# Performance work log

Measured on AMD Instinct MI355X. Metric: run time of the kernel, lower is better.

## Reference

```python
import jax, jax.numpy as jnp
import numpy as np

EMBED_DIM = 512
N_HEADS = 8
HEAD_DIM = EMBED_DIM // N_HEADS
SEQ = 4096
BATCH = 2


def setup_inputs() -> dict:
    key = jax.random.key(0)
    k1, k2, k3 = jax.random.split(key, 3)
    x = jax.random.normal(k1, (SEQ, BATCH, EMBED_DIM), dtype=jnp.float32)
    # xavier_uniform for [3E, E]: limit = sqrt(6/(3E+E))
    lim_in = float(np.sqrt(6.0 / (3 * EMBED_DIM + EMBED_DIM)))
    in_proj_weight = jax.random.uniform(k2, (3 * EMBED_DIM, EMBED_DIM), minval=-lim_in, maxval=lim_in, dtype=jnp.float32)
    in_proj_bias = jnp.zeros((3 * EMBED_DIM,), jnp.float32)
    lim_out = float(np.sqrt(1.0 / EMBED_DIM))  # torch Linear default init range
    out_weight = jax.random.uniform(k3, (EMBED_DIM, EMBED_DIM), minval=-lim_out, maxval=lim_out, dtype=jnp.float32)
    out_bias = jnp.zeros((EMBED_DIM,), jnp.float32)
    return {"x": x, "in_proj_weight": in_proj_weight, "in_proj_bias": in_proj_bias,
            "out_weight": out_weight, "out_bias": out_bias}


def reference(x, in_proj_weight, in_proj_bias, out_weight, out_bias):
    # x: [S, B, E] (seq-first, as in the torch module)
    S, B, E = x.shape
    H, D = N_HEADS, HEAD_DIM
    scaling = 1.0 / (D ** 0.5)
    qkv = x @ in_proj_weight.T + in_proj_bias            # [S, B, 3E]
    q, k, v = jnp.split(qkv, 3, axis=-1)                 # each [S, B, E]
    # reshape to [B*H, S, D]
    def to_bh(t):
        return t.reshape(S, B * H, D).transpose(1, 0, 2)
    q = to_bh(q * scaling)
    k = to_bh(k)
    v = to_bh(v)
    scores = jnp.einsum('bqd,bkd->bqk', q, k)            # [B*H, S, S]
    attn = jax.nn.softmax(scores, axis=-1)
    out = jnp.einsum('bqk,bkd->bqd', attn, v)            # [B*H, S, D]
    out = out.transpose(1, 0, 2).reshape(S, B, E)        # [S, B, E]
    return out @ out_weight.T + out_bias
```

## Files before the change

kernel.cpp:

```cpp
#include <hip/hip_runtime.h>

typedef unsigned short u16;
typedef unsigned int   u32;
typedef short bf16x8 __attribute__((ext_vector_type(8)));
typedef float f32x2  __attribute__((ext_vector_type(2)));
typedef float f32x4  __attribute__((ext_vector_type(4)));
typedef float f32x16 __attribute__((ext_vector_type(16)));
typedef u32   u32x4  __attribute__((ext_vector_type(4)));

#define QK_SCALE 0.18033688011112042f

__device__ __forceinline__ u16 f2bf(float f) {
  u32 u = __builtin_bit_cast(u32, f);
  u = (u + 0x7FFFu + ((u >> 16) & 1u)) >> 16;
  return (u16)u;
}

__device__ __forceinline__ u32 cvtpk(float lo, float hi) {
  u32 r;
  asm("v_cvt_pk_bf16_f32 %0, %1, %2" : "=v"(r) : "v"(lo), "v"(hi));
  return r;
}

__device__ __forceinline__ void gload16(void* lds, const void* g) {
  __builtin_amdgcn_global_load_lds(
      (const __attribute__((address_space(1))) u32*)g,
      (__attribute__((address_space(3))) u32*)lds, 16, 0, 0);
}

__device__ __forceinline__ bf16x8 ld8(const void* p) {
  return *(const bf16x8*)p;
}

__global__ __launch_bounds__(256) void cvt_kernel(
    const float* __restrict__ x, const float* __restrict__ w1,
    const float* __restrict__ w2,
    u16* __restrict__ xb, u16* __restrict__ wb, u16* __restrict__ ob) {
  int i = blockIdx.x * 256 + threadIdx.x;
  const float* src; u16* dst; int off;
  if (i < 1048576)            { src = x;  dst = xb; off = i; }
  else if (i < 1048576+196608){ src = w1; dst = wb; off = i - 1048576; }
  else                        { src = w2; dst = ob; off = i - 1245184; }
  float4 v = ((const float4*)src)[off];
  ushort4 o;
  o.x = f2bf(v.x); o.y = f2bf(v.y); o.z = f2bf(v.z); o.w = f2bf(v.w);
  ((ushort4*)dst)[off] = o;
}

template<int MODE>
__global__ __launch_bounds__(256, 2) void gemm_bt(
    const u16* __restrict__ A, const u16* __restrict__ Bm,
    const float* __restrict__ bias,
    u16* __restrict__ q_out, u16* __restrict__ k_out, u16* __restrict__ v_out,
    float* __restrict__ f_out, int M, int N, int K) {
  __shared__ __attribute__((aligned(16))) u16 As[128 * 64];
  __shared__ __attribute__((aligned(16))) u16 Bs[128 * 64];
  const int tid = threadIdx.x, lane = tid & 63, w = tid >> 6;
  const int wm = w >> 1, wn = w & 1;
  const int lo = lane & 15, hi = lane >> 4;
  const int m0 = blockIdx.x * 128, n0 = blockIdx.y * 128;
  f32x4 acc[4][4] = {};
  const int srow = lane >> 3;
  const int skc  = (lane & 7) ^ srow;
  const int nk = K >> 6;
  for (int kt = 0; kt < nk; ++kt) {
    __syncthreads();
    const int k0 = kt * 64;
#pragma unroll
    for (int c = 0; c < 4; ++c) {
      const int ch = w * 4 + c;
      const int row = ch * 8 + srow;
      gload16((char*)As + ch * 1024, A  + (size_t)(m0 + row) * K + k0 + skc * 8);
      gload16((char*)Bs + ch * 1024, Bm + (size_t)(n0 + row) * K + k0 + skc * 8);
    }
    __syncthreads();
#pragma unroll
    for (int kk = 0; kk < 2; ++kk) {
      bf16x8 af[4], bfr[4];
#pragma unroll
      for (int mi = 0; mi < 4; ++mi) {
        const int row = wm * 64 + mi * 16 + lo;
        const int kc = kk * 4 + hi;
        af[mi] = ld8((const char*)As + row * 128 + ((kc ^ (row & 7)) << 4));
      }
#pragma unroll
      for (int ni = 0; ni < 4; ++ni) {
        const int row = wn * 64 + ni * 16 + lo;
        const int kc = kk * 4 + hi;
        bfr[ni] = ld8((const char*)Bs + row * 128 + ((kc ^ (row & 7)) << 4));
      }
#pragma unroll
      for (int mi = 0; mi < 4; ++mi)
#pragma unroll
        for (int ni = 0; ni < 4; ++ni)
          acc[mi][ni] = __builtin_amdgcn_mfma_f32_16x16x32_bf16(
              af[mi], bfr[ni], acc[mi][ni], 0, 0, 0);
    }
  }
#pragma unroll
  for (int mi = 0; mi < 4; ++mi)
#pragma unroll
    for (int ni = 0; ni < 4; ++ni) {
      const int gn = n0 + wn * 64 + ni * 16 + lo;
      const float bv = bias[gn];
#pragma unroll
      for (int r = 0; r < 4; ++r) {
        const int gm = m0 + wm * 64 + mi * 16 + hi * 4 + r;
        float val = acc[mi][ni][r] + bv;
        if (MODE == 0) {
          const int s = gm >> 1, b = gm & 1;
          const int sec = gn >> 9, e = gn & 511;
          const int h = e >> 6, d = e & 63;
          const size_t o = (((size_t)(b * 8 + h) * 4096 + s) << 6) + d;
          if (sec == 0)      q_out[o] = f2bf(val * QK_SCALE);
          else if (sec == 1) k_out[o] = f2bf(val);
          else               v_out[o] = f2bf(val);
        } else {
          f_out[(size_t)gm * N + gn] = val;
        }
      }
    }
}

__global__ __launch_bounds__(256) void transpose_v(
    const u16* __restrict__ v, u16* __restrict__ vt) {
  __shared__ __attribute__((aligned(16))) u16 T[64 * 72];
  const int bh = blockIdx.y, s0 = blockIdx.x * 64;
  const int t = threadIdx.x;
#pragma unroll
  for (int i = 0; i < 2; ++i) {
    const int idx = t + i * 256;
    const int row = idx >> 3, c = idx & 7;
    uint4 d = *(const uint4*)(v + ((size_t)bh * 4096 + s0 + row) * 64 + c * 8);
    *(uint4*)(&T[row * 72 + c * 8]) = d;
  }
  __syncthreads();
#pragma unroll
  for (int i = 0; i < 2; ++i) {
    const int idx = t + i * 256;
    const int dcol = idx >> 3, sc = idx & 7;
    u16 tmp[8];
#pragma unroll
    for (int j = 0; j < 8; ++j) tmp[j] = T[(sc * 8 + j) * 72 + dcol];
    *(uint4*)(vt + ((size_t)bh * 64 + dcol) * 4096 + s0 + sc * 8) = *(const uint4*)tmp;
  }
}

__global__ __launch_bounds__(256, 2) void fa_kernel(
    const u16* __restrict__ q, const u16* __restrict__ k,
    const u16* __restrict__ vt, u16* __restrict__ attn) {
  __shared__ __attribute__((aligned(16))) char S_lds[2][2][16384];
  __shared__ float Ml[2][2][32];
  const int tid = threadIdx.x, lane = tid & 63, w = tid >> 6;
  const int lo = lane & 31, hi5 = lane >> 5;
  const int wq = w & 1;
  const int kvh = w >> 1;
  const int wg = blockIdx.x;
  const int xcd = wg & 7, idx = wg >> 3;
  const int bh = xcd * 2 + (idx >> 5), qb = idx & 31;
  const int q0 = qb * 128 + wq * 64;
  const size_t hb = (size_t)bh * 4096 * 64;
  const u16* kbase = k + hb;
  const u16* vbase = vt + hb;
  bf16x8 qfA[4], qfB[4];
#pragma unroll
  for (int ds = 0; ds < 4; ++ds) {
    qfA[ds] = ld8(q + hb + (size_t)(q0 + lo) * 64 + ds * 16 + hi5 * 8);
    qfB[ds] = ld8(q + hb + (size_t)(q0 + 32 + lo) * 64 + ds * 16 + hi5 * 8);
  }

  f32x16 accA[2] = {}, accB[2] = {};
  float lrunA = 0.f, lrunB = 0.f;

  const int srow8 = lane >> 3;
  const int sx    = (lane & 7) ^ srow8;
  const int schunk = wq * 4;

#define STAGE(buf, kv0)                                                       \
  {                                                                           \
    char* kb_l = S_lds[kvh][buf];                                             \
    char* vb_l = kb_l + 8192;                                                 \
    _Pragma("unroll")                                                         \
    for (int i = 0; i < 4; ++i) {                                             \
      const int c = schunk + i;                       \
      gload16(kb_l + c * 1024,                                                \
              kbase + (size_t)((kv0) + c * 8 + srow8) * 64 + sx * 8);         \
      gload16(vb_l + c * 1024,                                                \
              vbase + (size_t)(c * 8 + srow8) * 4096 + (kv0) + sx * 8);       \
    }                                                                         \
  }

#define PACK(stv, ksl, pa)                                                    \
  {                                                                           \
    u32 A0 = cvtpk(stv[8 * ksl + 0], stv[8 * ksl + 1]);                       \
    u32 A1 = cvtpk(stv[8 * ksl + 2], stv[8 * ksl + 3]);                       \
    u32 B0 = cvtpk(stv[8 * ksl + 4], stv[8 * ksl + 5]);                       \
    u32 B1 = cvtpk(stv[8 * ksl + 6], stv[8 * ksl + 7]);                       \
    asm("v_permlane32_swap_b32 %0, %1" : "+v"(A0), "+v"(B0));                 \
    asm("v_permlane32_swap_b32 %0, %1" : "+v"(A1), "+v"(B1));                 \
    u32x4 pw; pw.x = A0; pw.y = A1; pw.z = B0; pw.w = B1;                     \
    pa = __builtin_bit_cast(bf16x8, pw);                                      \
  }

  const int kvbase = kvh * 2048;
  STAGE(0, kvbase);
  __syncthreads();

  for (int kb = 0; kb < 32; ++kb) {
    const int cur = kb & 1;
    if (kb < 31) STAGE(cur ^ 1, kvbase + (kb + 1) * 64);
    const char* kl = S_lds[kvh][cur];
    const char* vl = kl + 8192;
    f32x16 stA0 = {}, stA1 = {}, stB0 = {}, stB1 = {};
    __builtin_amdgcn_s_setprio(1);
#pragma unroll
    for (int ds = 0; ds < 4; ++ds) {
      const int r0 = lo, r1 = 32 + lo;
      const int col = ds * 32 + hi5 * 16;
      bf16x8 kf0 = ld8(kl + r0 * 128 + (col ^ ((r0 & 7) << 4)));
      bf16x8 kf1 = ld8(kl + r1 * 128 + (col ^ ((r1 & 7) << 4)));
      stA0 = __builtin_amdgcn_mfma_f32_32x32x16_bf16(kf0, qfA[ds], stA0, 0,0,0);
      stB0 = __builtin_amdgcn_mfma_f32_32x32x16_bf16(kf0, qfB[ds], stB0, 0,0,0);
      stA1 = __builtin_amdgcn_mfma_f32_32x32x16_bf16(kf1, qfA[ds], stA1, 0,0,0);
      stB1 = __builtin_amdgcn_mfma_f32_32x32x16_bf16(kf1, qfB[ds], stB1, 0,0,0);
    }
    __builtin_amdgcn_s_setprio(0);
    f32x2 ltA; ltA.x = 0.f; ltA.y = 0.f;
    f32x2 ltB; ltB.x = 0.f; ltB.y = 0.f;
#pragma unroll
    for (int i = 0; i < 8; ++i) {
      stA0[2*i]   = __builtin_amdgcn_exp2f(stA0[2*i]);
      stA0[2*i+1] = __builtin_amdgcn_exp2f(stA0[2*i+1]);
      f32x2 a0; a0.x = stA0[2*i]; a0.y = stA0[2*i+1]; ltA += a0;
      stA1[2*i]   = __builtin_amdgcn_exp2f(stA1[2*i]);
      stA1[2*i+1] = __builtin_amdgcn_exp2f(stA1[2*i+1]);
      f32x2 a1; a1.x = stA1[2*i]; a1.y = stA1[2*i+1]; ltA += a1;
      stB0[2*i]   = __builtin_amdgcn_exp2f(stB0[2*i]);
      stB0[2*i+1] = __builtin_amdgcn_exp2f(stB0[2*i+1]);
      f32x2 b0; b0.x = stB0[2*i]; b0.y = stB0[2*i+1]; ltB += b0;
      stB1[2*i]   = __builtin_amdgcn_exp2f(stB1[2*i]);
      stB1[2*i+1] = __builtin_amdgcn_exp2f(stB1[2*i+1]);
      f32x2 b1; b1.x = stB1[2*i]; b1.y = stB1[2*i+1]; ltB += b1;
    }
    lrunA += ltA.x + ltA.y;
    lrunB += ltB.x + ltB.y;
    __builtin_amdgcn_s_setprio(1);
#pragma unroll
    for (int h32 = 0; h32 < 2; ++h32) {
#pragma unroll
      for (int ksl = 0; ksl < 2; ++ksl) {
        bf16x8 paA, paB;
        if (h32 == 0) { PACK(stA0, ksl, paA); PACK(stB0, ksl, paB); }
        else          { PACK(stA1, ksl, paA); PACK(stB1, ksl, paB); }
#pragma unroll
        for (int ds2 = 0; ds2 < 2; ++ds2) {
          const int row = ds2 * 32 + lo;
          bf16x8 vf = ld8(vl + row * 128 +
                          ((h32 * 64 + ksl * 32 + hi5 * 16) ^ ((row & 7) << 4)));
          accA[ds2] = __builtin_amdgcn_mfma_f32_32x32x16_bf16(paA, vf,
                                                              accA[ds2], 0,0,0);
          accB[ds2] = __builtin_amdgcn_mfma_f32_32x32x16_bf16(paB, vf,
                                                              accB[ds2], 0,0,0);
        }
      }
    }
    __builtin_amdgcn_s_setprio(0);
    __syncthreads();
  }
  lrunA += __shfl_xor(lrunA, 32);
  lrunB += __shfl_xor(lrunB, 32);
  float* Ob = (float*)S_lds;
  if (w >= 2) {
#pragma unroll
    for (int r = 0; r < 16; ++r) {
      const int crow = (r & 3) + 8 * (r >> 2) + 4 * hi5;
#pragma unroll
      for (int ds2 = 0; ds2 < 2; ++ds2) {
        Ob[((wq * 2 + 0) * 32 + crow) * 64 + ds2 * 32 + lo] = accA[ds2][r];
        Ob[((wq * 2 + 1) * 32 + crow) * 64 + ds2 * 32 + lo] = accB[ds2][r];
      }
    }
    if (hi5 == 0) { Ml[wq][0][lo] = lrunA; Ml[wq][1][lo] = lrunB; }
  }
  __syncthreads();
  if (w < 2) {
    const float linvA = 1.0f / (lrunA + Ml[wq][0][lo]);
    const float linvB = 1.0f / (lrunB + Ml[wq][1][lo]);
    const int b = bh >> 3, h = bh & 7;
#pragma unroll
    for (int r = 0; r < 16; ++r) {
      const int crow = (r & 3) + 8 * (r >> 2) + 4 * hi5;
      const float ivA = __shfl(linvA, crow);
      const float ivB = __shfl(linvB, crow);
      const int sA = q0 + crow, sB = q0 + 32 + crow;
#pragma unroll
      for (int ds2 = 0; ds2 < 2; ++ds2) {
        const float oA = Ob[((wq * 2 + 0) * 32 + crow) * 64 + ds2 * 32 + lo];
        const float oB = Ob[((wq * 2 + 1) * 32 + crow) * 64 + ds2 * 32 + lo];
        attn[(size_t)(sA * 2 + b) * 512 + h * 64 + ds2 * 32 + lo] =
            f2bf((accA[ds2][r] + oA) * ivA);
        attn[(size_t)(sB * 2 + b) * 512 + h * 64 + ds2 * 32 + lo] =
            f2bf((accB[ds2][r] + oB) * ivB);
      }
    }
  }
#undef STAGE
#undef PACK
}

extern "C" void kernel_launch(void* const* d_in, const int* in_sizes, int n_in,
                              void* d_out, int out_size, void* d_ws, size_t ws_size,
                              hipStream_t stream) {
  const float* x     = (const float*)d_in[0];
  const float* w_in  = (const float*)d_in[1];
  const float* b_in  = (const float*)d_in[2];
  const float* w_out = (const float*)d_in[3];
  const float* b_out = (const float*)d_in[4];
  float* out = (float*)d_out;
  char* ws = (char*)d_ws;
  u16* xb  = (u16*)(ws);
  u16* wb  = (u16*)(ws + 8388608);
  u16* ob  = (u16*)(ws + 9961472);
  u16* qb  = (u16*)(ws + 10485760);
  u16* kb  = (u16*)(ws + 18874368);
  u16* vb  = (u16*)(ws + 27262976);
  u16* vtb = (u16*)(ws + 35651584);
  u16* attn = xb;

  cvt_kernel<<<5120, 256, 0, stream>>>(x, w_in, w_out, xb, wb, ob);
  gemm_bt<0><<<dim3(64, 12), 256, 0, stream>>>(xb, wb, b_in, qb, kb, vb,
                                               nullptr, 8192, 1536, 512);
  transpose_v<<<dim3(64, 16), 256, 0, stream>>>(vb, vtb);
  fa_kernel<<<512, 256, 0, stream>>>(qb, kb, vtb, attn);
  gemm_bt<1><<<dim3(64, 4), 256, 0, stream>>>(attn, ob, b_out, nullptr, nullptr,
                                              nullptr, out, 8192, 512, 512);
}
```

Before: 134.5 us.

## Software-pipeline attention loop: defer PV MFMAs to overlap next tile's QK and softmax

```diff
diff --git a/kernel.cpp b/kernel.cpp
--- a/kernel.cpp
+++ b/kernel.cpp
@@ -171,6 +171,8 @@
 
   f32x16 accA[2] = {}, accB[2] = {};
   float lrunA = 0.f, lrunB = 0.f;
+  bf16x8 paA[4], paB[4];
+  bf16x8 vfr[8];
 
   const int srow8 = lane >> 3;
   const int sx    = (lane & 7) ^ srow8;
@@ -202,71 +204,88 @@
     pa = __builtin_bit_cast(bf16x8, pw);                                      \
   }
 
+#define PVSTEP()                                                              \
+  {                                                                           \
+    __builtin_amdgcn_s_setprio(1);                                            \
+    _Pragma("unroll")                                                         \
+    for (int sl = 0; sl < 4; ++sl)                                            \
+      _Pragma("unroll")                                                       \
+      for (int ds2 = 0; ds2 < 2; ++ds2) {                                     \
+        accA[ds2] = __builtin_amdgcn_mfma_f32_32x32x16_bf16(                  \
+            paA[sl], vfr[sl * 2 + ds2], accA[ds2], 0, 0, 0);                  \
+        accB[ds2] = __builtin_amdgcn_mfma_f32_32x32x16_bf16(                  \
+            paB[sl], vfr[sl * 2 + ds2], accB[ds2], 0, 0, 0);                  \
+      }                                                                       \
+    __builtin_amdgcn_s_setprio(0);                                            \
+  }
+
+#define COMPUTE(CUR)                                                          \
+  {                                                                           \
+    const char* kl = S_lds[kvh][CUR];                                         \
+    const char* vl = kl + 8192;                                               \
+    f32x16 stA0 = {}, stA1 = {}, stB0 = {}, stB1 = {};                        \
+    __builtin_amdgcn_s_setprio(1);                                            \
+    _Pragma("unroll")                                                         \
+    for (int ds = 0; ds < 4; ++ds) {                                          \
+      const int r0 = lo, r1 = 32 + lo;                                        \
+      const int col = ds * 32 + hi5 * 16;                                     \
+      bf16x8 kf0 = ld8(kl + r0 * 128 + (col ^ ((r0 & 7) << 4)));              \
+      bf16x8 kf1 = ld8(kl + r1 * 128 + (col ^ ((r1 & 7) << 4)));              \
+      stA0 = __builtin_amdgcn_mfma_f32_32x32x16_bf16(kf0, qfA[ds], stA0,0,0,0);\
+      stB0 = __builtin_amdgcn_mfma_f32_32x32x16_bf16(kf0, qfB[ds], stB0,0,0,0);\
+      stA1 = __builtin_amdgcn_mfma_f32_32x32x16_bf16(kf1, qfA[ds], stA1,0,0,0);\
+      stB1 = __builtin_amdgcn_mfma_f32_32x32x16_bf16(kf1, qfB[ds], stB1,0,0,0);\
+    }                                                                         \
+    __builtin_amdgcn_s_setprio(0);                                            \
+    _Pragma("unroll")                                                         \
+    for (int sl = 0; sl < 4; ++sl)                                            \
+      _Pragma("unroll")                                                       \
+      for (int ds2 = 0; ds2 < 2; ++ds2) {                                     \
+        const int row = ds2 * 32 + lo;                                        \
+        vfr[sl * 2 + ds2] = ld8(vl + row * 128 +                              \
+                                ((sl * 32 + hi5 * 16) ^ ((row & 7) << 4)));   \
+      }                                                                       \
+    f32x2 ltA; ltA.x = 0.f; ltA.y = 0.f;                                      \
+    f32x2 ltB; ltB.x = 0.f; ltB.y = 0.f;                                      \
+    _Pragma("unroll")                                                         \
+    for (int i = 0; i < 8; ++i) {                                             \
+      stA0[2*i]   = __builtin_amdgcn_exp2f(stA0[2*i]);                        \
+      stA0[2*i+1] = __builtin_amdgcn_exp2f(stA0[2*i+1]);                      \
+      f32x2 a0; a0.x = stA0[2*i]; a0.y = stA0[2*i+1]; ltA += a0;              \
+      stA1[2*i]   = __builtin_amdgcn_exp2f(stA1[2*i]);                        \
+      stA1[2*i+1] = __builtin_amdgcn_exp2f(stA1[2*i+1]);                      \
+      f32x2 a1; a1.x = stA1[2*i]; a1.y = stA1[2*i+1]; ltA += a1;              \
+      stB0[2*i]   = __builtin_amdgcn_exp2f(stB0[2*i]);                        \
+      stB0[2*i+1] = __builtin_amdgcn_exp2f(stB0[2*i+1]);                      \
+      f32x2 b0; b0.x = stB0[2*i]; b0.y = stB0[2*i+1]; ltB += b0;              \
+      stB1[2*i]   = __builtin_amdgcn_exp2f(stB1[2*i]);                        \
+      stB1[2*i+1] = __builtin_amdgcn_exp2f(stB1[2*i+1]);                      \
+      f32x2 b1; b1.x = stB1[2*i]; b1.y = stB1[2*i+1]; ltB += b1;              \
+    }                                                                         \
+    lrunA += ltA.x + ltA.y;                                                   \
+    lrunB += ltB.x + ltB.y;                                                   \
+    PACK(stA0, 0, paA[0]); PACK(stA0, 1, paA[1]);                             \
+    PACK(stA1, 0, paA[2]); PACK(stA1, 1, paA[3]);                             \
+    PACK(stB0, 0, paB[0]); PACK(stB0, 1, paB[1]);                             \
+    PACK(stB1, 0, paB[2]); PACK(stB1, 1, paB[3]);                             \
+  }
+
   const int kvbase = kvh * 2048;
   STAGE(0, kvbase);
   __syncthreads();
-
-  for (int kb = 0; kb < 32; ++kb) {
-    const int cur = kb & 1;
-    if (kb < 31) STAGE(cur ^ 1, kvbase + (kb + 1) * 64);
-    const char* kl = S_lds[kvh][cur];
-    const char* vl = kl + 8192;
-    f32x16 stA0 = {}, stA1 = {}, stB0 = {}, stB1 = {};
-    __builtin_amdgcn_s_setprio(1);
-#pragma unroll
-    for (int ds = 0; ds < 4; ++ds) {
-      const int r0 = lo, r1 = 32 + lo;
-      const int col = ds * 32 + hi5 * 16;
-      bf16x8 kf0 = ld8(kl + r0 * 128 + (col ^ ((r0 & 7) << 4)));
-      bf16x8 kf1 = ld8(kl + r1 * 128 + (col ^ ((r1 & 7) << 4)));
-      stA0 = __builtin_amdgcn_mfma_f32_32x32x16_bf16(kf0, qfA[ds], stA0, 0,0,0);
-      stB0 = __builtin_amdgcn_mfma_f32_32x32x16_bf16(kf0, qfB[ds], stB0, 0,0,0);
-      stA1 = __builtin_amdgcn_mfma_f32_32x32x16_bf16(kf1, qfA[ds], stA1, 0,0,0);
-      stB1 = __builtin_amdgcn_mfma_f32_32x32x16_bf16(kf1, qfB[ds], stB1, 0,0,0);
-    }
-    __builtin_amdgcn_s_setprio(0);
-    f32x2 ltA; ltA.x = 0.f; ltA.y = 0.f;
-    f32x2 ltB; ltB.x = 0.f; ltB.y = 0.f;
-#pragma unroll
-    for (int i = 0; i < 8; ++i) {
-      stA0[2*i]   = __builtin_amdgcn_exp2f(stA0[2*i]);
-      stA0[2*i+1] = __builtin_amdgcn_exp2f(stA0[2*i+1]);
-      f32x2 a0; a0.x = stA0[2*i]; a0.y = stA0[2*i+1]; ltA += a0;
-      stA1[2*i]   = __builtin_amdgcn_exp2f(stA1[2*i]);
-      stA1[2*i+1] = __builtin_amdgcn_exp2f(stA1[2*i+1]);
-      f32x2 a1; a1.x = stA1[2*i]; a1.y = stA1[2*i+1]; ltA += a1;
-      stB0[2*i]   = __builtin_amdgcn_exp2f(stB0[2*i]);
-      stB0[2*i+1] = __builtin_amdgcn_exp2f(stB0[2*i+1]);
-      f32x2 b0; b0.x = stB0[2*i]; b0.y = stB0[2*i+1]; ltB += b0;
-      stB1[2*i]   = __builtin_amdgcn_exp2f(stB1[2*i]);
-      stB1[2*i+1] = __builtin_amdgcn_exp2f(stB1[2*i+1]);
-      f32x2 b1; b1.x = stB1[2*i]; b1.y = stB1[2*i+1]; ltB += b1;
-    }
-    lrunA += ltA.x + ltA.y;
-    lrunB += ltB.x + ltB.y;
-    __builtin_amdgcn_s_setprio(1);
-#pragma unroll
-    for (int h32 = 0; h32 < 2; ++h32) {
-#pragma unroll
-      for (int ksl = 0; ksl < 2; ++ksl) {
-        bf16x8 paA, paB;
-        if (h32 == 0) { PACK(stA0, ksl, paA); PACK(stB0, ksl, paB); }
-        else          { PACK(stA1, ksl, paA); PACK(stB1, ksl, paB); }
-#pragma unroll
-        for (int ds2 = 0; ds2 < 2; ++ds2) {
-          const int row = ds2 * 32 + lo;
-          bf16x8 vf = ld8(vl + row * 128 +
-                          ((h32 * 64 + ksl * 32 + hi5 * 16) ^ ((row & 7) << 4)));
-          accA[ds2] = __builtin_amdgcn_mfma_f32_32x32x16_bf16(paA, vf,
-                                                              accA[ds2], 0,0,0);
-          accB[ds2] = __builtin_amdgcn_mfma_f32_32x32x16_bf16(paB, vf,
-                                                              accB[ds2], 0,0,0);
-        }
-      }
-    }
-    __builtin_amdgcn_s_setprio(0);
+  STAGE(1, kvbase + 64);
+  COMPUTE(0);
+  __syncthreads();
+
+  for (int t = 1; t < 32; ++t) {
+    const int cur = t & 1;
+    if (t < 31) STAGE(cur ^ 1, kvbase + (t + 1) * 64);
+    PVSTEP();
+    if (cur) { COMPUTE(1); } else { COMPUTE(0); }
     __syncthreads();
   }
+  PVSTEP();
+
   lrunA += __shfl_xor(lrunA, 32);
   lrunB += __shfl_xor(lrunB, 32);
   float* Ob = (float*)S_lds;
@@ -306,6 +325,8 @@
   }
 #undef STAGE
 #undef PACK
+#undef PVSTEP
+#undef COMPUTE
 }
 
 extern "C" void kernel_launch(void* const* d_in, const int* in_sizes, int n_in,
```

New measurement: 132.4 us, median of 2. No clear change (-1.5%).
